# Kernel tuning notes

Hardware: AMD Instinct MI355X
Metric: run time of the kernel (lower is better)

Reference implementation:

```python
import jax, jax.numpy as jnp
import numpy as np

TEMPERATURE = 0.07
BASE_TEMPERATURE = 0.07


def _pairwise_euclid(x):
    # torch.cdist(x, x, p=2), with safe sqrt (zero grad at zero distance)
    sq = jnp.sum(x * x, axis=1)
    d2 = sq[:, None] + sq[None, :] - 2.0 * (x @ x.T)
    d2 = jnp.maximum(d2, 0.0)
    safe = jnp.where(d2 > 0.0, d2, 1.0)
    return jnp.where(d2 > 0.0, jnp.sqrt(safe), 0.0)


def setup_inputs() -> dict:
    key = jax.random.key(0)
    k1, k2 = jax.random.split(key)
    features = jax.random.normal(k1, (1024, 2, 512), dtype=jnp.float32)
    labels = jax.random.uniform(k2, (1024,), dtype=jnp.float32)
    return {"features": features, "labels": labels}


def reference(features, labels):
    B, V, D = features.shape
    N = B * V
    # torch.cat(torch.unbind(features, dim=1), dim=0): views stacked -> [N, D]
    cf = features.transpose(1, 0, 2).reshape(N, D)
    lab = jnp.tile(labels, V)  # label of row i is labels[i % B]

    dist = _pairwise_euclid(cf)              # [N, N]
    logits = -dist / TEMPERATURE
    eye = jnp.eye(N, dtype=logits.dtype)
    w = jnp.exp(logits) * (1.0 - eye)        # exp(logits) with l == i excluded

    dis = jnp.abs(lab[:, None] - lab[None, :])  # |y_i - y_j|, symmetric

    # negative[i, j] = sum_{l != i, |y_l - y_i| >= |y_i - y_j|} exp(logits[i, l])
    # computed per-row via sort + suffix cumsum + searchsorted (O(N^2 log N))
    order = jnp.argsort(dis, axis=1)
    sorted_d = jnp.take_along_axis(dis, order, axis=1)
    sorted_w = jnp.take_along_axis(w, order, axis=1)
    suffix = jnp.flip(jnp.cumsum(jnp.flip(sorted_w, axis=1), axis=1), axis=1)
    suffix = jnp.concatenate([suffix, jnp.zeros((N, 1), suffix.dtype)], axis=1)  # [N, N+1]
    # side='left': counts entries strictly < d, so suffix[idx] sums all >= d (ties incl.)
    idx = jax.vmap(lambda sd, d: jnp.searchsorted(sd, d, side='left'))(sorted_d, dis)
    negative = jnp.take_along_axis(suffix, idx, axis=1)
    negative = negative * (1.0 - eye) + eye  # diag set to 1 (log -> 0)

    logits_z = logits * (1.0 - eye)          # logits[i, i] = 0
    log_prob = logits_z - jnp.log(negative)
    mean_log_prob_pos = jnp.sum(log_prob, axis=1) / (N - 1)
    loss = -(TEMPERATURE / BASE_TEMPERATURE) * jnp.mean(mean_log_prob_pos)
    return loss
```

## Files before the change

### kernel.cpp

```cpp
#include <hip/hip_runtime.h>
#include <math.h>


#define NN 2048
#define BB 1024
#define DD 512
#define NT 256
#define NEGINF (-INFINITY)
#define CS 64.0f

typedef short s16x8 __attribute__((ext_vector_type(8)));
typedef float f32x4 __attribute__((ext_vector_type(4)));

__device__ __forceinline__ const float* cf_row(const float* F, int i) {
    return F + ((size_t)(i & (BB - 1)) * 2 + (size_t)(i >> 10)) * DD;
}

__device__ __forceinline__ unsigned bf_rne(float x) {
    const unsigned u = __float_as_uint(x);
    return (u + 0x7FFFu + ((u >> 16) & 1u)) >> 16;
}
__device__ __forceinline__ float bf_val(unsigned h) {
    return __uint_as_float(h << 16);
}

__global__ __launch_bounds__(512) void sort_labels_kernel(const float* __restrict__ labels,
                                                          float* __restrict__ slab,
                                                          int* __restrict__ sj) {
    __shared__ float kk[BB];
    __shared__ int   id[BB];
    const int t = threadIdx.x;
    #pragma unroll
    for (int e = 0; e < 2; ++e) { const int p = t + e * 512; kk[p] = labels[p]; id[p] = p; }
    for (int k = 2; k <= BB; k <<= 1) {
        for (int j = k >> 1; j > 0; j >>= 1) {
            if (j >= 32) __syncthreads();
            else __builtin_amdgcn_wave_barrier();
            #pragma unroll
            for (int e = 0; e < 2; ++e) {
                const int idx = t + e * 512;
                const int ixj = idx ^ j;
                if (ixj > idx) {
                    const float k1 = kk[idx], k2 = kk[ixj];
                    const bool up = ((idx & k) == 0);
                    if (up ? (k1 > k2) : (k1 < k2)) {
                        kk[idx] = k2; kk[ixj] = k1;
                        const int i1 = id[idx]; id[idx] = id[ixj]; id[ixj] = i1;
                    }
                }
            }
        }
    }
    __syncthreads();
    #pragma unroll
    for (int e = 0; e < 2; ++e) {
        const int p = t + e * 512;
        const float lv = kk[p];
        const int b = id[p];
        slab[2 * p] = lv; slab[2 * p + 1] = lv;
        sj[2 * p] = b;    sj[2 * p + 1] = b + BB;
    }
}

__global__ __launch_bounds__(256) void prep_split_kernel(const float* __restrict__ F,
                                                         ushort* __restrict__ Ahi,
                                                         ushort* __restrict__ Alo,
                                                         float* __restrict__ sq) {
    const int t = threadIdx.x;
    const int lane = t & 63;
    const int w = t >> 6;
    const int i = blockIdx.x * 4 + w;
    const float* src = cf_row(F, i);
    const float4 v0 = reinterpret_cast<const float4*>(src)[lane];
    const float4 v1 = reinterpret_cast<const float4*>(src)[lane + 64];
    float ss = v0.x * v0.x + v0.y * v0.y + v0.z * v0.z + v0.w * v0.w
             + v1.x * v1.x + v1.y * v1.y + v1.z * v1.z + v1.w * v1.w;
    #pragma unroll
    for (int st = 32; st > 0; st >>= 1) ss += __shfl_down(ss, st);
    if (lane == 0) sq[i] = ss;

    const float a[8] = {v0.x, v0.y, v0.z, v0.w, v1.x, v1.y, v1.z, v1.w};
    ushort h[8], l[8];
    #pragma unroll
    for (int e = 0; e < 8; ++e) {
        const unsigned hb = bf_rne(a[e]);
        h[e] = (ushort)hb;
        l[e] = (ushort)bf_rne(a[e] - bf_val(hb));
    }
    const size_t base = (size_t)i * DD;
    *reinterpret_cast<ushort4*>(&Ahi[base + lane * 4])       = make_ushort4(h[0], h[1], h[2], h[3]);
    *reinterpret_cast<ushort4*>(&Ahi[base + 256 + lane * 4]) = make_ushort4(h[4], h[5], h[6], h[7]);
    *reinterpret_cast<ushort4*>(&Alo[base + lane * 4])       = make_ushort4(l[0], l[1], l[2], l[3]);
    *reinterpret_cast<ushort4*>(&Alo[base + 256 + lane * 4]) = make_ushort4(l[4], l[5], l[6], l[7]);
}

#define TM 128
#define TN 64
#define TK 32
__global__ __launch_bounds__(256) void gemm_dist_kernel(const ushort* __restrict__ Ahi,
                                                        const ushort* __restrict__ Alo,
                                                        const float* __restrict__ sq,
                                                        const int* __restrict__ sj,
                                                        float* __restrict__ distp) {
    __shared__ ushort Ah[4][TM][8];
    __shared__ ushort Al[4][TM][8];
    __shared__ ushort Bh[4][TN][8];
    __shared__ ushort Bl[4][TN][8];
    __shared__ int   sjcA[TM];
    __shared__ int   sjcB[TN];
    __shared__ float sqA[TM];
    __shared__ float sqB[TN];

    const int t = threadIdx.x;
    const int lane = t & 63;
    const int w = t >> 6;

    const int id = blockIdx.x;
    int by = (int)((__fsqrt_rn(4.0f * (float)id + 1.0f) - 1.0f) * 0.5f);
    while ((by + 1) * (by + 2) <= id) ++by;
    while (by * (by + 1) > id) --by;
    const int bx = id - by * (by + 1);
    const int row0 = by * TM;
    const int col0 = bx * TN;
    const bool below = (bx < 2 * by);

    if (t < TM) {
        const int s = sj[row0 + t];
        sjcA[t] = s; sqA[t] = sq[s];
    } else if (t < TM + TN) {
        const int u = t - TM;
        const int s = sj[col0 + u];
        sjcB[u] = s; sqB[u] = sq[s];
    }
    __syncthreads();
    const int rr = t >> 2;
    const int cq = t & 3;
    const size_t gA0 = (size_t)sjcA[rr] * DD + cq * 8;
    const size_t gA1 = (size_t)sjcA[64 + rr] * DD + cq * 8;
    const size_t gB0 = (size_t)sjcB[rr] * DD + cq * 8;

    f32x4 acc[2][4] = {};
    const int m = lane & 15;
    const int q = lane >> 4;

    for (int kt = 0; kt < DD / TK; ++kt) {
        __syncthreads();
        const size_t ko = (size_t)kt * TK;
        *reinterpret_cast<int4*>(&Ah[cq][rr][0])      = *reinterpret_cast<const int4*>(&Ahi[gA0 + ko]);
        *reinterpret_cast<int4*>(&Al[cq][rr][0])      = *reinterpret_cast<const int4*>(&Alo[gA0 + ko]);
        *reinterpret_cast<int4*>(&Ah[cq][64 + rr][0]) = *reinterpret_cast<const int4*>(&Ahi[gA1 + ko]);
        *reinterpret_cast<int4*>(&Al[cq][64 + rr][0]) = *reinterpret_cast<const int4*>(&Alo[gA1 + ko]);
        *reinterpret_cast<int4*>(&Bh[cq][rr][0])      = *reinterpret_cast<const int4*>(&Ahi[gB0 + ko]);
        *reinterpret_cast<int4*>(&Bl[cq][rr][0])      = *reinterpret_cast<const int4*>(&Alo[gB0 + ko]);
        __syncthreads();

        s16x8 fah[2], fal[2], fbh[4], fbl[4];
        #pragma unroll
        for (int mt = 0; mt < 2; ++mt) {
            fah[mt] = *reinterpret_cast<const s16x8*>(&Ah[q][w * 32 + mt * 16 + m][0]);
            fal[mt] = *reinterpret_cast<const s16x8*>(&Al[q][w * 32 + mt * 16 + m][0]);
        }
        #pragma unroll
        for (int nt = 0; nt < 4; ++nt) {
            fbh[nt] = *reinterpret_cast<const s16x8*>(&Bh[q][nt * 16 + m][0]);
            fbl[nt] = *reinterpret_cast<const s16x8*>(&Bl[q][nt * 16 + m][0]);
        }
        #pragma unroll
        for (int mt = 0; mt < 2; ++mt)
            #pragma unroll
            for (int nt = 0; nt < 4; ++nt) {
                acc[mt][nt] = __builtin_amdgcn_mfma_f32_16x16x32_bf16(fah[mt], fbh[nt], acc[mt][nt], 0, 0, 0);
                acc[mt][nt] = __builtin_amdgcn_mfma_f32_16x16x32_bf16(fah[mt], fbl[nt], acc[mt][nt], 0, 0, 0);
                acc[mt][nt] = __builtin_amdgcn_mfma_f32_16x16x32_bf16(fal[mt], fbh[nt], acc[mt][nt], 0, 0, 0);
            }
    }

    #pragma unroll
    for (int mt = 0; mt < 2; ++mt) {
        const int lr0 = w * 32 + mt * 16 + q * 4;
        #pragma unroll
        for (int nt = 0; nt < 4; ++nt) {
            const int lc = nt * 16 + m;
            float o[4];
            #pragma unroll
            for (int r = 0; r < 4; ++r) {
                const float d2 = sqA[lr0 + r] + sqB[lc] - 2.0f * acc[mt][nt][r];
                o[r] = (d2 > 0.f) ? sqrtf(d2) : 0.f;
            }
            #pragma unroll
            for (int r = 0; r < 4; ++r)
                distp[(size_t)(row0 + lr0 + r) * NN + col0 + lc] = o[r];
            if (below) {
                const float4 o4 = make_float4(o[0], o[1], o[2], o[3]);
                *reinterpret_cast<float4*>(&distp[(size_t)(col0 + lc) * NN + row0 + lr0]) = o4;
            }
        }
    }
}

__device__ __forceinline__ int bs_right(const float* key, float d, int lo, int hi) {
    while (lo < hi) {
        const int mid = (lo + hi) >> 1;
        if (key[mid] >= d) hi = mid; else lo = mid + 1;
    }
    return lo;
}
__device__ __forceinline__ int bs_left(const float* key, float d, int lo, int hi) {
    while (lo < hi) {
        const int mid = (lo + hi) >> 1;
        if (key[mid] < d) hi = mid; else lo = mid + 1;
    }
    return lo;
}

__global__ __launch_bounds__(256) void row_kernel(const float* __restrict__ distp,
                                                  const float* __restrict__ slab,
                                                  double* __restrict__ rowval) {
    __shared__ float key[NN];
    __shared__ float Pf[NN];
    __shared__ float Sf[NN + 1];
    __shared__ float wmxA[4], wmxB[4], wps[4], wss[4];
    __shared__ double wDA[4], wLA[4], wDB[4], wLB[4];

    const int pr = blockIdx.x;
    const int rA = 2 * pr, rB = 2 * pr + 1;
    const int t = threadIdx.x;
    const int lane = t & 63;
    const int w = t >> 6;
    const float x = slab[rA];
    const float negInvT = -1.0f / 0.07f;
    const float* drowA = &distp[(size_t)rA * NN];
    const float* drowB = &distp[(size_t)rB * NN];

    #pragma unroll
    for (int e = 0; e < 2; ++e) {
        const int p4 = t + e * NT;
        const float4 l4 = reinterpret_cast<const float4*>(slab)[p4];
        key[p4 * 4 + 0] = fabsf(l4.x - x);
        key[p4 * 4 + 1] = fabsf(l4.y - x);
        key[p4 * 4 + 2] = fabsf(l4.z - x);
        key[p4 * 4 + 3] = fabsf(l4.w - x);
    }
    const int cb = t * 8;
    float vA[8], vB[8];
    double dsumA = 0.0, dsumB = 0.0;
    float mxA = NEGINF, mxB = NEGINF;
    #pragma unroll
    for (int e = 0; e < 2; ++e) {
        const float4 a4 = reinterpret_cast<const float4*>(drowA)[2 * t + e];
        const float4 b4 = reinterpret_cast<const float4*>(drowB)[2 * t + e];
        const float av[4] = {a4.x, a4.y, a4.z, a4.w};
        const float bv[4] = {b4.x, b4.y, b4.z, b4.w};
        #pragma unroll
        for (int c = 0; c < 4; ++c) {
            const int pc = cb + e * 4 + c;
            if (pc == rA) vA[e * 4 + c] = NEGINF;
            else { const float vv = av[c] * negInvT; vA[e * 4 + c] = vv; mxA = fmaxf(mxA, vv); dsumA += (double)av[c]; }
            if (pc == rB) vB[e * 4 + c] = NEGINF;
            else { const float vv = bv[c] * negInvT; vB[e * 4 + c] = vv; mxB = fmaxf(mxB, vv); dsumB += (double)bv[c]; }
        }
    }
    #pragma unroll
    for (int st = 32; st > 0; st >>= 1) {
        mxA = fmaxf(mxA, __shfl_down(mxA, st));
        mxB = fmaxf(mxB, __shfl_down(mxB, st));
    }
    if (lane == 0) { wmxA[w] = mxA; wmxB[w] = mxB; }
    __syncthreads();
    const float MA = fmaxf(fmaxf(wmxA[0], wmxA[1]), fmaxf(wmxA[2], wmxA[3]));
    const float MB = fmaxf(fmaxf(wmxB[0], wmxB[1]), fmaxf(wmxB[2], wmxB[3]));

    int L8[8], R8[8];
    const int a = cb, b = cb + 7;
    {
        const int le = (rA - 1 < b) ? rA - 1 : b;
        if (a <= le) {
            const float da = key[a];
            const int Ra = bs_right(key, da, rA, NN);
            int Rl = Ra;
            if (le > a) Rl = bs_right(key, key[le], rA, Ra);
            for (int p = a; p <= le; ++p) {
                const float d = key[p];
                int R;
                if (p == a) R = Ra;
                else if (p == le) R = Rl;
                else R = bs_right(key, d, Rl, Ra);
                int L = p + 1;
                while (L < rA && key[L] == d) ++L;
                L8[p - a] = L; R8[p - a] = R;
            }
        }
        const int rs = (rA + 1 > a) ? rA + 1 : a;
        if (rs <= b) {
            const float dr = key[rs];
            const int Lr = bs_left(key, dr, 0, rA);
            int Lb = Lr;
            if (b > rs) Lb = bs_left(key, key[b], 0, Lr);
            for (int p = rs; p <= b; ++p) {
                const float d = key[p];
                int L;
                if (p == rs) L = Lr;
                else if (p == b) L = Lb;
                else L = bs_left(key, d, Lb, Lr);
                int R = p;
                while (R > rA && key[R - 1] == d) --R;
                L8[p - a] = L; R8[p - a] = R;
            }
        }
        if (rA >= a && rA <= b) { L8[rA - a] = rA; R8[rA - a] = rA; }
    }

    double lnsumA = 0.0;
    {
        float e8[8];
        #pragma unroll
        for (int jj = 0; jj < 8; ++jj) e8[jj] = __expf(vA[jj] - MA + CS);
        {
            float run = 0.f, ex[8];
            #pragma unroll
            for (int jj = 0; jj < 8; ++jj) { ex[jj] = run; run += e8[jj]; }
            float inc = run;
            #pragma unroll
            for (int st = 1; st < 64; st <<= 1) {
                const float nm = __shfl_up(inc, st);
                if (lane >= st) inc += nm;
            }
            float xofs = __shfl_up(inc, 1);
            if (lane == 0) xofs = 0.f;
            if (lane == 63) wps[w] = inc;
            __syncthreads();
            #pragma unroll
            for (int ww = 0; ww < 3; ++ww)
                if (ww < w) xofs += wps[ww];
            #pragma unroll
            for (int jj = 0; jj < 8; ++jj) Pf[cb + jj] = ex[jj] + xofs;
        }
        {
            float run = 0.f, sx[8];
            #pragma unroll
            for (int jj = 7; jj >= 0; --jj) { run += e8[jj]; sx[jj] = run; }
            float inc = run;
            #pragma unroll
            for (int st = 1; st < 64; st <<= 1) {
                const float nm = __shfl_down(inc, st);
                if (lane + st < 64) inc += nm;
            }
            float xofs = __shfl_down(inc, 1);
            if (lane == 63) xofs = 0.f;
            if (lane == 0) wss[w] = inc;
            __syncthreads();
            #pragma unroll
            for (int ww = 1; ww < 4; ++ww)
                if (ww > w) xofs += wss[ww];
            #pragma unroll
            for (int jj = 0; jj < 8; ++jj) Sf[cb + jj] = sx[jj] + xofs;
            if (t == 0) Sf[NN] = 0.f;
        }
        __syncthreads();
        const float MBA = MA - CS;
        #pragma unroll
        for (int jj = 0; jj < 8; ++jj) {
            const int p = cb + jj;
            if (p == rA) continue;
            const float s = fmaxf(Pf[L8[jj]] + Sf[R8[jj]], 1e-38f);
            lnsumA += (double)(MBA + __logf(s));
        }
    }
    __syncthreads();

    double lnsumB = 0.0;
    {
        float e8[8];
        #pragma unroll
        for (int jj = 0; jj < 8; ++jj) e8[jj] = __expf(vB[jj] - MB + CS);
        {
            float run = 0.f, ex[8];
            #pragma unroll
            for (int jj = 0; jj < 8; ++jj) { ex[jj] = run; run += e8[jj]; }
            float inc = run;
            #pragma unroll
            for (int st = 1; st < 64; st <<= 1) {
                const float nm = __shfl_up(inc, st);
                if (lane >= st) inc += nm;
            }
            float xofs = __shfl_up(inc, 1);
            if (lane == 0) xofs = 0.f;
            if (lane == 63) wps[w] = inc;
            __syncthreads();
            #pragma unroll
            for (int ww = 0; ww < 3; ++ww)
                if (ww < w) xofs += wps[ww];
            #pragma unroll
            for (int jj = 0; jj < 8; ++jj) Pf[cb + jj] = ex[jj] + xofs;
        }
        {
            float run = 0.f, sx[8];
            #pragma unroll
            for (int jj = 7; jj >= 0; --jj) { run += e8[jj]; sx[jj] = run; }
            float inc = run;
            #pragma unroll
            for (int st = 1; st < 64; st <<= 1) {
                const float nm = __shfl_down(inc, st);
                if (lane + st < 64) inc += nm;
            }
            float xofs = __shfl_down(inc, 1);
            if (lane == 63) xofs = 0.f;
            if (lane == 0) wss[w] = inc;
            __syncthreads();
            #pragma unroll
            for (int ww = 1; ww < 4; ++ww)
                if (ww > w) xofs += wss[ww];
            #pragma unroll
            for (int jj = 0; jj < 8; ++jj) Sf[cb + jj] = sx[jj] + xofs;
            if (t == 0) Sf[NN] = 0.f;
        }
        __syncthreads();
        const float MBB = MB - CS;
        #pragma unroll
        for (int jj = 0; jj < 8; ++jj) {
            const int p = cb + jj;
            if (p == rB) continue;
            const float s = fmaxf(Pf[L8[jj]] + Sf[R8[jj]], 1e-38f);
            lnsumB += (double)(MBB + __logf(s));
        }
    }

    #pragma unroll
    for (int st = 32; st > 0; st >>= 1) {
        dsumA  += __shfl_down(dsumA, st);
        lnsumA += __shfl_down(lnsumA, st);
        dsumB  += __shfl_down(dsumB, st);
        lnsumB += __shfl_down(lnsumB, st);
    }
    if (lane == 0) { wDA[w] = dsumA; wLA[w] = lnsumA; wDB[w] = dsumB; wLB[w] = lnsumB; }
    __syncthreads();
    if (t == 0) {
        rowval[rA] = (-(wDA[0] + wDA[1] + wDA[2] + wDA[3]) / 0.07)
                   - (wLA[0] + wLA[1] + wLA[2] + wLA[3]);
        rowval[rB] = (-(wDB[0] + wDB[1] + wDB[2] + wDB[3]) / 0.07)
                   - (wLB[0] + wLB[1] + wLB[2] + wLB[3]);
    }
}

__global__ __launch_bounds__(256) void finalize_kernel(const double* __restrict__ rowval,
                                                       float* __restrict__ out) {
    __shared__ double red[NT];
    const int t = threadIdx.x;
    double s = 0.0;
    for (int j = t; j < NN; j += NT) s += rowval[j];
    red[t] = s;
    __syncthreads();
    for (int ofs = NT / 2; ofs > 0; ofs >>= 1) {
        if (t < ofs) red[t] += red[t + ofs];
        __syncthreads();
    }
    if (t == 0) {
        out[0] = (float)(-red[0] / ((double)NN * (double)(NN - 1)));
    }
}

extern "C" void kernel_launch(void* const* d_in, const int* in_sizes, int n_in,
                              void* d_out, int out_size, void* d_ws, size_t ws_size,
                              hipStream_t stream) {
    const float* features = (const float*)d_in[0];
    const float* labels   = (const float*)d_in[1];
    float* out = (float*)d_out;

    char* ws = (char*)d_ws;
    size_t off = 0;
    float*  sq     = (float*) (ws + off); off += NN * sizeof(float);
    float*  slab   = (float*) (ws + off); off += NN * sizeof(float);
    int*    sj     = (int*)   (ws + off); off += NN * sizeof(int);
    double* rowval = (double*)(ws + off); off += NN * sizeof(double);
    ushort* Ahi    = (ushort*)(ws + off); off += (size_t)NN * DD * sizeof(ushort);
    ushort* Alo    = (ushort*)(ws + off); off += (size_t)NN * DD * sizeof(ushort);
    float*  distp  = (float*) (ws + off); off += (size_t)NN * NN * sizeof(float);

    sort_labels_kernel<<<1, 512, 0, stream>>>(labels, slab, sj);
    prep_split_kernel<<<NN / 4, NT, 0, stream>>>(features, Ahi, Alo, sq);
    gemm_dist_kernel<<<16 * 17, NT, 0, stream>>>(Ahi, Alo, sq, sj, distp);
    row_kernel<<<NN / 2, NT, 0, stream>>>(distp, slab, rowval);
    finalize_kernel<<<1, NT, 0, stream>>>(rowval, out);
}
```

Baseline: 134.2 us.

## Fuse label ranking into prep, retile GEMM to 64x64, fold finalize into row kernel

Replaces the single-block bitonic label sort with a rank-by-counting sort done by extra blocks of the feature prep kernel, so sorting runs in parallel with the bf16 split. The distance GEMM switches from 128x64 tiles to symmetric 64x64 lower-triangle tiles, giving 528 blocks instead of 272 for better occupancy. The finalize kernel is removed; row blocks atomically add their values into a double accumulator, and the last block (tracked with a counter) writes the loss. This cuts two launches but adds atomics and a 64-tile GEMM with less register reuse per block.

```diff
diff --git a/kernel.cpp b/kernel.cpp
--- a/kernel.cpp
+++ b/kernel.cpp
@@ -6,6 +6,7 @@
 #define BB 1024
 #define DD 512
 #define NT 256
+#define NPREP 512
 #define NEGINF (-INFINITY)
 #define CS 64.0f
 
@@ -24,176 +25,153 @@
     return __uint_as_float(h << 16);
 }
 
-__global__ __launch_bounds__(512) void sort_labels_kernel(const float* __restrict__ labels,
-                                                          float* __restrict__ slab,
-                                                          int* __restrict__ sj) {
-    __shared__ float kk[BB];
-    __shared__ int   id[BB];
+__global__ __launch_bounds__(256) void prep_kernel(const float* __restrict__ F,
+                                                   const float* __restrict__ labels,
+                                                   ushort* __restrict__ Ahi,
+                                                   ushort* __restrict__ Alo,
+                                                   float* __restrict__ sq,
+                                                   float* __restrict__ slab,
+                                                   int* __restrict__ sj,
+                                                   double* __restrict__ accum,
+                                                   unsigned* __restrict__ cnt) {
     const int t = threadIdx.x;
-    #pragma unroll
-    for (int e = 0; e < 2; ++e) { const int p = t + e * 512; kk[p] = labels[p]; id[p] = p; }
-    for (int k = 2; k <= BB; k <<= 1) {
-        for (int j = k >> 1; j > 0; j >>= 1) {
-            if (j >= 32) __syncthreads();
-            else __builtin_amdgcn_wave_barrier();
-            #pragma unroll
-            for (int e = 0; e < 2; ++e) {
-                const int idx = t + e * 512;
-                const int ixj = idx ^ j;
-                if (ixj > idx) {
-                    const float k1 = kk[idx], k2 = kk[ixj];
-                    const bool up = ((idx & k) == 0);
-                    if (up ? (k1 > k2) : (k1 < k2)) {
-                        kk[idx] = k2; kk[ixj] = k1;
-                        const int i1 = id[idx]; id[idx] = id[ixj]; id[ixj] = i1;
-                    }
-                }
-            }
-        }
-    }
-    __syncthreads();
-    #pragma unroll
-    for (int e = 0; e < 2; ++e) {
-        const int p = t + e * 512;
-        const float lv = kk[p];
-        const int b = id[p];
-        slab[2 * p] = lv; slab[2 * p + 1] = lv;
-        sj[2 * p] = b;    sj[2 * p + 1] = b + BB;
-    }
-}
-
-__global__ __launch_bounds__(256) void prep_split_kernel(const float* __restrict__ F,
-                                                         ushort* __restrict__ Ahi,
-                                                         ushort* __restrict__ Alo,
-                                                         float* __restrict__ sq) {
-    const int t = threadIdx.x;
-    const int lane = t & 63;
-    const int w = t >> 6;
-    const int i = blockIdx.x * 4 + w;
-    const float* src = cf_row(F, i);
-    const float4 v0 = reinterpret_cast<const float4*>(src)[lane];
-    const float4 v1 = reinterpret_cast<const float4*>(src)[lane + 64];
-    float ss = v0.x * v0.x + v0.y * v0.y + v0.z * v0.z + v0.w * v0.w
-             + v1.x * v1.x + v1.y * v1.y + v1.z * v1.z + v1.w * v1.w;
-    #pragma unroll
-    for (int st = 32; st > 0; st >>= 1) ss += __shfl_down(ss, st);
-    if (lane == 0) sq[i] = ss;
-
-    const float a[8] = {v0.x, v0.y, v0.z, v0.w, v1.x, v1.y, v1.z, v1.w};
-    ushort h[8], l[8];
-    #pragma unroll
-    for (int e = 0; e < 8; ++e) {
-        const unsigned hb = bf_rne(a[e]);
-        h[e] = (ushort)hb;
-        l[e] = (ushort)bf_rne(a[e] - bf_val(hb));
-    }
-    const size_t base = (size_t)i * DD;
-    *reinterpret_cast<ushort4*>(&Ahi[base + lane * 4])       = make_ushort4(h[0], h[1], h[2], h[3]);
-    *reinterpret_cast<ushort4*>(&Ahi[base + 256 + lane * 4]) = make_ushort4(h[4], h[5], h[6], h[7]);
-    *reinterpret_cast<ushort4*>(&Alo[base + lane * 4])       = make_ushort4(l[0], l[1], l[2], l[3]);
-    *reinterpret_cast<ushort4*>(&Alo[base + 256 + lane * 4]) = make_ushort4(l[4], l[5], l[6], l[7]);
-}
-
-#define TM 128
-#define TN 64
+    if (blockIdx.x < NPREP) {
+        const int lane = t & 63;
+        const int w = t >> 6;
+        const int i = blockIdx.x * 4 + w;
+        const float* src = cf_row(F, i);
+        const float4 v0 = reinterpret_cast<const float4*>(src)[lane];
+        const float4 v1 = reinterpret_cast<const float4*>(src)[lane + 64];
+        float ss = v0.x * v0.x + v0.y * v0.y + v0.z * v0.z + v0.w * v0.w
+                 + v1.x * v1.x + v1.y * v1.y + v1.z * v1.z + v1.w * v1.w;
+        #pragma unroll
+        for (int st = 32; st > 0; st >>= 1) ss += __shfl_down(ss, st);
+        if (lane == 0) sq[i] = ss;
+
+        const float a[8] = {v0.x, v0.y, v0.z, v0.w, v1.x, v1.y, v1.z, v1.w};
+        ushort h[8], l[8];
+        #pragma unroll
+        for (int e = 0; e < 8; ++e) {
+            const unsigned hb = bf_rne(a[e]);
+            h[e] = (ushort)hb;
+            l[e] = (ushort)bf_rne(a[e] - bf_val(hb));
+        }
+        const size_t base = (size_t)i * DD;
+        *reinterpret_cast<ushort4*>(&Ahi[base + lane * 4])       = make_ushort4(h[0], h[1], h[2], h[3]);
+        *reinterpret_cast<ushort4*>(&Ahi[base + 256 + lane * 4]) = make_ushort4(h[4], h[5], h[6], h[7]);
+        *reinterpret_cast<ushort4*>(&Alo[base + lane * 4])       = make_ushort4(l[0], l[1], l[2], l[3]);
+        *reinterpret_cast<ushort4*>(&Alo[base + 256 + lane * 4]) = make_ushort4(l[4], l[5], l[6], l[7]);
+    } else {
+        __shared__ float lab[BB];
+        #pragma unroll
+        for (int e = 0; e < 4; ++e) lab[t + e * NT] = labels[t + e * NT];
+        __syncthreads();
+        const int p = (blockIdx.x - NPREP) * NT + t;
+        const float L = lab[p];
+        int rank = 0;
+        #pragma unroll 4
+        for (int q4 = 0; q4 < BB / 4; ++q4) {
+            const float4 l4 = reinterpret_cast<const float4*>(lab)[q4];
+            const int q = q4 * 4;
+            rank += (l4.x < L) || (l4.x == L && (q + 0) < p);
+            rank += (l4.y < L) || (l4.y == L && (q + 1) < p);
+            rank += (l4.z < L) || (l4.z == L && (q + 2) < p);
+            rank += (l4.w < L) || (l4.w == L && (q + 3) < p);
+        }
+        slab[2 * rank] = L; slab[2 * rank + 1] = L;
+        sj[2 * rank] = p;   sj[2 * rank + 1] = p + BB;
+        if (blockIdx.x == NPREP && t == 0) { *accum = 0.0; *cnt = 0u; }
+    }
+}
+
+#define GT 64
 #define TK 32
 __global__ __launch_bounds__(256) void gemm_dist_kernel(const ushort* __restrict__ Ahi,
                                                         const ushort* __restrict__ Alo,
                                                         const float* __restrict__ sq,
                                                         const int* __restrict__ sj,
                                                         float* __restrict__ distp) {
-    __shared__ ushort Ah[4][TM][8];
-    __shared__ ushort Al[4][TM][8];
-    __shared__ ushort Bh[4][TN][8];
-    __shared__ ushort Bl[4][TN][8];
-    __shared__ int   sjcA[TM];
-    __shared__ int   sjcB[TN];
-    __shared__ float sqA[TM];
-    __shared__ float sqB[TN];
+    __shared__ ushort Ah[4][GT][8];
+    __shared__ ushort Al[4][GT][8];
+    __shared__ ushort Bh[4][GT][8];
+    __shared__ ushort Bl[4][GT][8];
+    __shared__ int   sjcA[GT];
+    __shared__ int   sjcB[GT];
+    __shared__ float sqA[GT];
+    __shared__ float sqB[GT];
 
     const int t = threadIdx.x;
     const int lane = t & 63;
     const int w = t >> 6;
 
     const int id = blockIdx.x;
-    int by = (int)((__fsqrt_rn(4.0f * (float)id + 1.0f) - 1.0f) * 0.5f);
-    while ((by + 1) * (by + 2) <= id) ++by;
-    while (by * (by + 1) > id) --by;
-    const int bx = id - by * (by + 1);
-    const int row0 = by * TM;
-    const int col0 = bx * TN;
-    const bool below = (bx < 2 * by);
-
-    if (t < TM) {
+    int by = (int)((__fsqrt_rn(8.0f * (float)id + 1.0f) - 1.0f) * 0.5f);
+    while ((by + 1) * (by + 2) / 2 <= id) ++by;
+    while (by * (by + 1) / 2 > id) --by;
+    const int bx = id - by * (by + 1) / 2;
+    const int row0 = by * GT;
+    const int col0 = bx * GT;
+    const bool diag = (bx == by);
+
+    if (t < GT) {
         const int s = sj[row0 + t];
         sjcA[t] = s; sqA[t] = sq[s];
-    } else if (t < TM + TN) {
-        const int u = t - TM;
+    } else if (t < 2 * GT) {
+        const int u = t - GT;
         const int s = sj[col0 + u];
         sjcB[u] = s; sqB[u] = sq[s];
     }
     __syncthreads();
     const int rr = t >> 2;
     const int cq = t & 3;
-    const size_t gA0 = (size_t)sjcA[rr] * DD + cq * 8;
-    const size_t gA1 = (size_t)sjcA[64 + rr] * DD + cq * 8;
-    const size_t gB0 = (size_t)sjcB[rr] * DD + cq * 8;
-
-    f32x4 acc[2][4] = {};
+    const size_t gA = (size_t)sjcA[rr] * DD + cq * 8;
+    const size_t gB = (size_t)sjcB[rr] * DD + cq * 8;
+
+    f32x4 acc[4] = {};
     const int m = lane & 15;
     const int q = lane >> 4;
 
     for (int kt = 0; kt < DD / TK; ++kt) {
         __syncthreads();
         const size_t ko = (size_t)kt * TK;
-        *reinterpret_cast<int4*>(&Ah[cq][rr][0])      = *reinterpret_cast<const int4*>(&Ahi[gA0 + ko]);
-        *reinterpret_cast<int4*>(&Al[cq][rr][0])      = *reinterpret_cast<const int4*>(&Alo[gA0 + ko]);
-        *reinterpret_cast<int4*>(&Ah[cq][64 + rr][0]) = *reinterpret_cast<const int4*>(&Ahi[gA1 + ko]);
-        *reinterpret_cast<int4*>(&Al[cq][64 + rr][0]) = *reinterpret_cast<const int4*>(&Alo[gA1 + ko]);
-        *reinterpret_cast<int4*>(&Bh[cq][rr][0])      = *reinterpret_cast<const int4*>(&Ahi[gB0 + ko]);
-        *reinterpret_cast<int4*>(&Bl[cq][rr][0])      = *reinterpret_cast<const int4*>(&Alo[gB0 + ko]);
+        *reinterpret_cast<int4*>(&Ah[cq][rr][0]) = *reinterpret_cast<const int4*>(&Ahi[gA + ko]);
+        *reinterpret_cast<int4*>(&Al[cq][rr][0]) = *reinterpret_cast<const int4*>(&Alo[gA + ko]);
+        *reinterpret_cast<int4*>(&Bh[cq][rr][0]) = *reinterpret_cast<const int4*>(&Ahi[gB + ko]);
+        *reinterpret_cast<int4*>(&Bl[cq][rr][0]) = *reinterpret_cast<const int4*>(&Alo[gB + ko]);
         __syncthreads();
 
-        s16x8 fah[2], fal[2], fbh[4], fbl[4];
-        #pragma unroll
-        for (int mt = 0; mt < 2; ++mt) {
-            fah[mt] = *reinterpret_cast<const s16x8*>(&Ah[q][w * 32 + mt * 16 + m][0]);
-            fal[mt] = *reinterpret_cast<const s16x8*>(&Al[q][w * 32 + mt * 16 + m][0]);
-        }
+        const s16x8 fah = *reinterpret_cast<const s16x8*>(&Ah[q][w * 16 + m][0]);
+        const s16x8 fal = *reinterpret_cast<const s16x8*>(&Al[q][w * 16 + m][0]);
+        s16x8 fbh[4], fbl[4];
         #pragma unroll
         for (int nt = 0; nt < 4; ++nt) {
             fbh[nt] = *reinterpret_cast<const s16x8*>(&Bh[q][nt * 16 + m][0]);
             fbl[nt] = *reinterpret_cast<const s16x8*>(&Bl[q][nt * 16 + m][0]);
         }
         #pragma unroll
-        for (int mt = 0; mt < 2; ++mt)
-            #pragma unroll
-            for (int nt = 0; nt < 4; ++nt) {
-                acc[mt][nt] = __builtin_amdgcn_mfma_f32_16x16x32_bf16(fah[mt], fbh[nt], acc[mt][nt], 0, 0, 0);
-                acc[mt][nt] = __builtin_amdgcn_mfma_f32_16x16x32_bf16(fah[mt], fbl[nt], acc[mt][nt], 0, 0, 0);
-                acc[mt][nt] = __builtin_amdgcn_mfma_f32_16x16x32_bf16(fal[mt], fbh[nt], acc[mt][nt], 0, 0, 0);
-            }
-    }
-
+        for (int nt = 0; nt < 4; ++nt) {
+            acc[nt] = __builtin_amdgcn_mfma_f32_16x16x32_bf16(fah, fbh[nt], acc[nt], 0, 0, 0);
+            acc[nt] = __builtin_amdgcn_mfma_f32_16x16x32_bf16(fah, fbl[nt], acc[nt], 0, 0, 0);
+            acc[nt] = __builtin_amdgcn_mfma_f32_16x16x32_bf16(fal, fbh[nt], acc[nt], 0, 0, 0);
+        }
+    }
+
+    const int lr0 = w * 16 + q * 4;
     #pragma unroll
-    for (int mt = 0; mt < 2; ++mt) {
-        const int lr0 = w * 32 + mt * 16 + q * 4;
-        #pragma unroll
-        for (int nt = 0; nt < 4; ++nt) {
-            const int lc = nt * 16 + m;
-            float o[4];
-            #pragma unroll
-            for (int r = 0; r < 4; ++r) {
-                const float d2 = sqA[lr0 + r] + sqB[lc] - 2.0f * acc[mt][nt][r];
-                o[r] = (d2 > 0.f) ? sqrtf(d2) : 0.f;
-            }
-            #pragma unroll
-            for (int r = 0; r < 4; ++r)
-                distp[(size_t)(row0 + lr0 + r) * NN + col0 + lc] = o[r];
-            if (below) {
-                const float4 o4 = make_float4(o[0], o[1], o[2], o[3]);
-                *reinterpret_cast<float4*>(&distp[(size_t)(col0 + lc) * NN + row0 + lr0]) = o4;
-            }
+    for (int nt = 0; nt < 4; ++nt) {
+        const int lc = nt * 16 + m;
+        float o[4];
+        #pragma unroll
+        for (int r = 0; r < 4; ++r) {
+            const float d2 = sqA[lr0 + r] + sqB[lc] - 2.0f * acc[nt][r];
+            o[r] = (d2 > 0.f) ? sqrtf(d2) : 0.f;
+        }
+        #pragma unroll
+        for (int r = 0; r < 4; ++r)
+            distp[(size_t)(row0 + lr0 + r) * NN + col0 + lc] = o[r];
+        if (!diag) {
+            const float4 o4 = make_float4(o[0], o[1], o[2], o[3]);
+            *reinterpret_cast<float4*>(&distp[(size_t)(col0 + lc) * NN + row0 + lr0]) = o4;
         }
     }
 }
@@ -215,7 +193,9 @@
 
 __global__ __launch_bounds__(256) void row_kernel(const float* __restrict__ distp,
                                                   const float* __restrict__ slab,
-                                                  double* __restrict__ rowval) {
+                                                  double* __restrict__ accum,
+                                                  unsigned* __restrict__ cnt,
+                                                  float* __restrict__ out) {
     __shared__ float key[NN];
     __shared__ float Pf[NN];
     __shared__ float Sf[NN + 1];
@@ -435,27 +415,17 @@
     if (lane == 0) { wDA[w] = dsumA; wLA[w] = lnsumA; wDB[w] = dsumB; wLB[w] = lnsumB; }
     __syncthreads();
     if (t == 0) {
-        rowval[rA] = (-(wDA[0] + wDA[1] + wDA[2] + wDA[3]) / 0.07)
-                   - (wLA[0] + wLA[1] + wLA[2] + wLA[3]);
-        rowval[rB] = (-(wDB[0] + wDB[1] + wDB[2] + wDB[3]) / 0.07)
-                   - (wLB[0] + wLB[1] + wLB[2] + wLB[3]);
-    }
-}
-
-__global__ __launch_bounds__(256) void finalize_kernel(const double* __restrict__ rowval,
-                                                       float* __restrict__ out) {
-    __shared__ double red[NT];
-    const int t = threadIdx.x;
-    double s = 0.0;
-    for (int j = t; j < NN; j += NT) s += rowval[j];
-    red[t] = s;
-    __syncthreads();
-    for (int ofs = NT / 2; ofs > 0; ofs >>= 1) {
-        if (t < ofs) red[t] += red[t + ofs];
-        __syncthreads();
-    }
-    if (t == 0) {
-        out[0] = (float)(-red[0] / ((double)NN * (double)(NN - 1)));
+        const double rowA = (-(wDA[0] + wDA[1] + wDA[2] + wDA[3]) / 0.07)
+                          - (wLA[0] + wLA[1] + wLA[2] + wLA[3]);
+        const double rowB = (-(wDB[0] + wDB[1] + wDB[2] + wDB[3]) / 0.07)
+                          - (wLB[0] + wLB[1] + wLB[2] + wLB[3]);
+        atomicAdd(accum, rowA + rowB);
+        __threadfence();
+        const unsigned old = atomicAdd(cnt, 1u);
+        if (old == (unsigned)(gridDim.x - 1)) {
+            const double tot = atomicAdd(accum, 0.0);
+            out[0] = (float)(-tot / ((double)NN * (double)(NN - 1)));
+        }
     }
 }
 
@@ -467,18 +437,17 @@
     float* out = (float*)d_out;
 
     char* ws = (char*)d_ws;
-    size_t off = 0;
-    float*  sq     = (float*) (ws + off); off += NN * sizeof(float);
-    float*  slab   = (float*) (ws + off); off += NN * sizeof(float);
-    int*    sj     = (int*)   (ws + off); off += NN * sizeof(int);
-    double* rowval = (double*)(ws + off); off += NN * sizeof(double);
-    ushort* Ahi    = (ushort*)(ws + off); off += (size_t)NN * DD * sizeof(ushort);
-    ushort* Alo    = (ushort*)(ws + off); off += (size_t)NN * DD * sizeof(ushort);
-    float*  distp  = (float*) (ws + off); off += (size_t)NN * NN * sizeof(float);
-
-    sort_labels_kernel<<<1, 512, 0, stream>>>(labels, slab, sj);
-    prep_split_kernel<<<NN / 4, NT, 0, stream>>>(features, Ahi, Alo, sq);
-    gemm_dist_kernel<<<16 * 17, NT, 0, stream>>>(Ahi, Alo, sq, sj, distp);
-    row_kernel<<<NN / 2, NT, 0, stream>>>(distp, slab, rowval);
-    finalize_kernel<<<1, NT, 0, stream>>>(rowval, out);
-}
+    double*   accum = (double*)  (ws + 0);
+    unsigned* cnt   = (unsigned*)(ws + 8);
+    float*    sq    = (float*)   (ws + 64);
+    float*    slab  = (float*)   (ws + 64 + 8192);
+    int*      sj    = (int*)     (ws + 64 + 16384);
+    ushort*   Ahi   = (ushort*)  (ws + 24640);
+    ushort*   Alo   = (ushort*)  (ws + 24640 + (size_t)NN * DD * 2);
+    float*    distp = (float*)   (ws + 24640 + (size_t)NN * DD * 4);
+
+    prep_kernel<<<NPREP + 4, NT, 0, stream>>>(features, labels, Ahi, Alo, sq,
+                                              slab, sj, accum, cnt);
+    gemm_dist_kernel<<<32 * 33 / 2, NT, 0, stream>>>(Ahi, Alo, sq, sj, distp);
+    row_kernel<<<NN / 2, NT, 0, stream>>>(distp, slab, accum, cnt, out);
+}
```

Result: slower. 149.0 us (+11.0%).
